# Kernel tuning notes

Hardware: AMD Instinct MI355X
Metric: run time of the kernel (lower is better)

The kernel has to match this reference:

```python
import jax, jax.numpy as jnp
import numpy as np

B, C, H, W = 16, 256, 64, 64
NH, HD, NM = 4, 32, 4  # heads, head_dim, memory tokens
HID = NH * HD


def rms_norm(x, g):
    # F.normalize(x, dim=1) * sqrt(C) * g  (channel dim = 1)
    norm = jnp.maximum(jnp.linalg.norm(x, axis=1, keepdims=True), 1e-12)
    return x / norm * (x.shape[1] ** 0.5) * g


def setup_inputs() -> dict:
    key = jax.random.key(0)
    ks = jax.random.split(key, 5)
    return {
        "x": jax.random.normal(ks[0], (B, C, H, W), jnp.float32),
        "g_in": jnp.ones((1, C, 1, 1), jnp.float32),
        "mem_kv": jax.random.normal(ks[1], (2, NH, HD, NM), jnp.float32),
        "w_qkv": jax.random.normal(ks[2], (HID * 3, C), jnp.float32) * (C ** -0.5),
        "w_out": jax.random.normal(ks[3], (C, HID), jnp.float32) * (HID ** -0.5),
        "b_out": jnp.zeros((C,), jnp.float32),
        "g_out": jnp.ones((1, C, 1, 1), jnp.float32),
    }


def reference(x, g_in, mem_kv, w_qkv, w_out, b_out, g_out):
    b, c, h, w = x.shape
    n = h * w
    scale = HD ** -0.5

    xn = rms_norm(x, g_in)
    # 1x1 conv as matmul over channel dim: [B, 3*HID, H, W]
    qkv = jnp.einsum('oc,bchw->bohw', w_qkv, xn)
    q, k, v = jnp.split(qkv, 3, axis=1)
    # b (h d) x y -> b h d n
    q = q.reshape(b, NH, HD, n)
    k = k.reshape(b, NH, HD, n)
    v = v.reshape(b, NH, HD, n)

    # prepend memory key/value tokens: [b, h, d, NM + n]
    mk = jnp.broadcast_to(mem_kv[0], (b, NH, HD, NM))
    mv = jnp.broadcast_to(mem_kv[1], (b, NH, HD, NM))
    k = jnp.concatenate([mk, k], axis=-1)
    v = jnp.concatenate([mv, v], axis=-1)

    q = jax.nn.softmax(q, axis=-2) * scale  # softmax over head_dim
    k = jax.nn.softmax(k, axis=-1)          # softmax over tokens

    context = jnp.einsum('bhdn,bhen->bhde', k, v)  # [b, h, d, e]
    out = jnp.einsum('bhde,bhdn->bhen', context, q)  # [b, h, e, n]
    out = out.reshape(b, HID, h, w)

    out = jnp.einsum('oc,bchw->bohw', w_out, out) + b_out[None, :, None, None]
    return rms_norm(out, g_out)
```

## Files before the change

kernel.cpp:

```cpp
#include <hip/hip_runtime.h>
#include <math.h>

typedef unsigned short u16;
typedef unsigned int u32;

#define NBATCH 16
#define NCH    256
#define NPIX   4096
#define NHEAD  4
#define HDIM   32
#define NMEM   4
#define HID    128
#define OC3    384
#define SCALE_Q 0.17677669529663687f

typedef __bf16 bf16x8 __attribute__((ext_vector_type(8)));
typedef float  f32x4  __attribute__((ext_vector_type(4)));

__device__ __forceinline__ float bf2f(u16 u){ return __uint_as_float(((u32)u)<<16); }
__device__ __forceinline__ u16 f2bf(float f){
  u32 x = __float_as_uint(f);
  x += 0x7fffu + ((x>>16)&1u);
  return (u16)(x>>16);
}
__device__ __forceinline__ void unpack8(int4 v, float* o){
  u32 a=(u32)v.x, b=(u32)v.y, c=(u32)v.z, d=(u32)v.w;
  o[0]=__uint_as_float(a<<16); o[1]=__uint_as_float(a&0xffff0000u);
  o[2]=__uint_as_float(b<<16); o[3]=__uint_as_float(b&0xffff0000u);
  o[4]=__uint_as_float(c<<16); o[5]=__uint_as_float(c&0xffff0000u);
  o[6]=__uint_as_float(d<<16); o[7]=__uint_as_float(d&0xffff0000u);
}

__global__ __launch_bounds__(256) void k_pack(const float* __restrict__ wqkv,
                                              const float* __restrict__ gin,
                                              const float* __restrict__ wout,
                                              u16* __restrict__ wqb,
                                              u16* __restrict__ wob)
{
  int i = blockIdx.x*256 + threadIdx.x;
  if (i < OC3*NCH){ int c = i & 255; wqb[i] = f2bf(wqkv[i]*gin[c]); }
  else { int j = i - OC3*NCH; wob[j] = f2bf(wout[j]); }
}

__global__ __launch_bounds__(512) void k_qkvx(const float* __restrict__ x,
                                              const u16* __restrict__ wqb,
                                              u16* __restrict__ qkv)
{
  __shared__ u16 BxDs[64*264];
  __shared__ float ssqp[8][64];
  __shared__ float rl[64];
  u16* Ds = BxDs;
  const int t = threadIdx.x, w = t>>6, lane = t&63;
  const int n0 = blockIdx.x*64, b = blockIdx.y;
  const int qw = lane>>4, rr = lane&15;

  {
    const float* xp = x + ((size_t)b*NCH + w*32)*NPIX + n0 + lane;
    float ssq = 0.f;
    #pragma unroll
    for (int j=0;j<4;j++){
      u32 pk[4];
      #pragma unroll
      for (int q=0;q<4;q++){
        float v0 = xp[(size_t)(j*8+2*q  )*NPIX];
        float v1 = xp[(size_t)(j*8+2*q+1)*NPIX];
        ssq += v0*v0 + v1*v1;
        pk[q] = (u32)f2bf(v0) | ((u32)f2bf(v1)<<16);
      }
      *(int4*)&BxDs[lane*264 + w*32 + j*8] = make_int4((int)pk[0],(int)pk[1],(int)pk[2],(int)pk[3]);
    }
    ssqp[w][lane] = ssq;
  }
  __syncthreads();
  if (t < 64){
    float s = 0.f;
    #pragma unroll
    for (int g=0;g<8;g++) s += ssqp[g][t];
    rl[t] = 16.0f / fmaxf(sqrtf(s), 1e-12f);
  }

  f32x4 acc[3][4];
  #pragma unroll
  for (int p=0;p<3;p++)
    #pragma unroll
    for (int nf=0;nf<4;nf++) acc[p][nf] = (f32x4){0.f,0.f,0.f,0.f};

  const u16* a0 = wqb + (size_t)(0*128 + w*16 + rr)*NCH + qw*8;
  const u16* a1 = wqb + (size_t)(1*128 + w*16 + rr)*NCH + qw*8;
  const u16* a2 = wqb + (size_t)(2*128 + w*16 + rr)*NCH + qw*8;
  #pragma unroll
  for (int c0=0; c0<NCH; c0+=32){
    bf16x8 af0 = *(const bf16x8*)(a0 + c0);
    bf16x8 af1 = *(const bf16x8*)(a1 + c0);
    bf16x8 af2 = *(const bf16x8*)(a2 + c0);
    bf16x8 bfr[4];
    #pragma unroll
    for (int nf=0;nf<4;nf++)
      bfr[nf] = *(const bf16x8*)&BxDs[(nf*16+rr)*264 + c0 + qw*8];
    #pragma unroll
    for (int nf=0;nf<4;nf++){
      acc[0][nf] = __builtin_amdgcn_mfma_f32_16x16x32_bf16(af0, bfr[nf], acc[0][nf], 0, 0, 0);
      acc[1][nf] = __builtin_amdgcn_mfma_f32_16x16x32_bf16(af1, bfr[nf], acc[1][nf], 0, 0, 0);
      acc[2][nf] = __builtin_amdgcn_mfma_f32_16x16x32_bf16(af2, bfr[nf], acc[2][nf], 0, 0, 0);
    }
  }

  for (int p=0;p<3;p++){
    __syncthreads();
    #pragma unroll
    for (int nf=0;nf<4;nf++){
      int col = nf*16 + rr;
      float rv = rl[col];
      #pragma unroll
      for (int reg=0;reg<4;reg++){
        int rowl = w*16 + qw*4 + reg;
        Ds[rowl*72 + col] = f2bf(acc[p][nf][reg] * rv);
      }
    }
    __syncthreads();
    if (p==0){
      if (t < 256){
        int h = t>>6, n = t&63;
        float v[32];
        float m = -1e30f;
        #pragma unroll
        for (int d=0;d<32;d++){ v[d] = bf2f(Ds[(h*32+d)*72 + n]); m = fmaxf(m, v[d]); }
        float s = 0.f;
        #pragma unroll
        for (int d=0;d<32;d++){ v[d] = __expf(v[d]-m); s += v[d]; }
        float inv = SCALE_Q / s;
        #pragma unroll
        for (int d=0;d<32;d++) Ds[(h*32+d)*72 + n] = f2bf(v[d]*inv);
      }
      __syncthreads();
    }
    int ro = t>>2, seg = (t&3)*16;
    u16* dst = qkv + ((size_t)(b*OC3 + p*128 + ro))*NPIX + n0 + seg;
    *(int4*)dst     = *(const int4*)&Ds[ro*72 + seg];
    *(int4*)(dst+8) = *(const int4*)&Ds[ro*72 + seg + 8];
  }
}

__global__ __launch_bounds__(256) void k_kred(const u16* __restrict__ qkv,
                                              const float* __restrict__ memkv,
                                              float2* __restrict__ kms,
                                              float* __restrict__ ksm)
{
  const int rid = blockIdx.x*4 + (threadIdx.x>>6);
  const int lane = threadIdx.x & 63;
  const int d = rid & 31, h = (rid>>5)&3, b = rid>>7;
  const u16* p = qkv + (size_t)(b*OC3 + HID + h*HDIM + d)*NPIX;
  u32 buf[32];
  #pragma unroll
  for (int j=0;j<8;j++)
    *(int4*)&buf[j*4] = *(const int4*)(p + (size_t)(j*64+lane)*8);
  float m = -1e30f;
  #pragma unroll
  for (int i=0;i<32;i++){
    float lo = __uint_as_float(buf[i]<<16);
    float hi = __uint_as_float(buf[i]&0xffff0000u);
    m = fmaxf(m, fmaxf(lo, hi));
  }
  float mv[4];
  #pragma unroll
  for (int mm=0;mm<4;mm++){ mv[mm] = memkv[(h*HDIM+d)*NMEM + mm]; m = fmaxf(m, mv[mm]); }
  #pragma unroll
  for (int sh=1; sh<64; sh<<=1) m = fmaxf(m, __shfl_xor(m, sh, 64));
  float ssum = 0.f;
  #pragma unroll
  for (int i=0;i<32;i++){
    float lo = __uint_as_float(buf[i]<<16);
    float hi = __uint_as_float(buf[i]&0xffff0000u);
    ssum += __expf(lo-m) + __expf(hi-m);
  }
  #pragma unroll
  for (int sh=1; sh<64; sh<<=1) ssum += __shfl_xor(ssum, sh, 64);
  #pragma unroll
  for (int mm=0;mm<4;mm++) ssum += __expf(mv[mm]-m);
  float inv = 1.0f/ssum;
  if (lane==0) kms[rid] = make_float2(m, inv);
  if (lane<4) ksm[rid*NMEM + lane] = __expf(mv[lane]-m)*inv;
}

__global__ __launch_bounds__(64) void k_ctx(const u16* __restrict__ qkv,
                                            const float* __restrict__ memkv,
                                            const float* __restrict__ ksm,
                                            const float2* __restrict__ kms,
                                            float* __restrict__ ctxp)
{
  __shared__ float Ks[32][132];
  __shared__ float Vs[32][132];
  const int bh = blockIdx.x;
  const int s  = blockIdx.y;
  const int b = bh>>2, h = bh&3;
  const int t = threadIdx.x;
  const int d0 = (t>>3)*4, e0 = (t&7)*4;
  float acc[4][4] = {};
  if (s==0){
    #pragma unroll
    for (int m=0;m<4;m++){
      float km[4];
      #pragma unroll
      for (int pi=0;pi<4;pi++) km[pi] = ksm[(bh*HDIM + d0+pi)*NMEM + m];
      #pragma unroll
      for (int q=0;q<4;q++){
        float vm = memkv[((NHEAD+h)*HDIM + e0+q)*NMEM + m];
        #pragma unroll
        for (int pi=0;pi<4;pi++) acc[pi][q] += km[pi]*vm;
      }
    }
  }
  const u16* kb = qkv + (size_t)(b*OC3 +   HID + h*HDIM)*NPIX;
  const u16* vb = qkv + (size_t)(b*OC3 + 2*HID + h*HDIM)*NPIX;
  const int lr = t>>1, lseg = (t&1)*64;
  const float2 ms = kms[bh*HDIM + lr];
  const int n0 = s*128;
  {
    const u16* kp = kb + (size_t)lr*NPIX + n0 + lseg;
    const u16* vp = vb + (size_t)lr*NPIX + n0 + lseg;
    #pragma unroll
    for (int u=0;u<8;u++){
      int4 kv = *(const int4*)(kp + u*8);
      int4 vv = *(const int4*)(vp + u*8);
      float kf[8], vf[8];
      unpack8(kv,kf); unpack8(vv,vf);
      #pragma unroll
      for (int i=0;i<8;i++) kf[i] = __expf(kf[i]-ms.x)*ms.y;
      *(float4*)&Ks[lr][lseg+u*8]   = make_float4(kf[0],kf[1],kf[2],kf[3]);
      *(float4*)&Ks[lr][lseg+u*8+4] = make_float4(kf[4],kf[5],kf[6],kf[7]);
      *(float4*)&Vs[lr][lseg+u*8]   = make_float4(vf[0],vf[1],vf[2],vf[3]);
      *(float4*)&Vs[lr][lseg+u*8+4] = make_float4(vf[4],vf[5],vf[6],vf[7]);
    }
    __syncthreads();
    #pragma unroll 4
    for (int nn=0;nn<128;nn+=4){
      float kq[4][4] __attribute__((aligned(16)));
      float vq[4][4] __attribute__((aligned(16)));
      #pragma unroll
      for (int pi=0;pi<4;pi++) *(float4*)kq[pi] = *(const float4*)&Ks[d0+pi][nn];
      #pragma unroll
      for (int q=0;q<4;q++)    *(float4*)vq[q]  = *(const float4*)&Vs[e0+q][nn];
      #pragma unroll
      for (int pi=0;pi<4;pi++)
        #pragma unroll
        for (int q=0;q<4;q++)
          acc[pi][q] += kq[pi][0]*vq[q][0] + kq[pi][1]*vq[q][1]
                      + kq[pi][2]*vq[q][2] + kq[pi][3]*vq[q][3];
    }
  }
  #pragma unroll
  for (int pi=0;pi<4;pi++)
    *(float4*)(ctxp + (size_t)(s*64+bh)*1024 + (d0+pi)*32 + e0) =
      make_float4(acc[pi][0],acc[pi][1],acc[pi][2],acc[pi][3]);
}

__global__ __launch_bounds__(256) void k_ctxred(const float* __restrict__ ctxp,
                                                float* __restrict__ ctx)
{
  const int bh = blockIdx.x, t = threadIdx.x;
  float4 s = make_float4(0.f,0.f,0.f,0.f);
  #pragma unroll
  for (int sp=0; sp<32; sp++){
    float4 v = *(const float4*)(ctxp + (size_t)(sp*64+bh)*1024 + t*4);
    s.x+=v.x; s.y+=v.y; s.z+=v.z; s.w+=v.w;
  }
  *(float4*)(ctx + (size_t)bh*1024 + t*4) = s;
}

__global__ __launch_bounds__(256) void k_fout(const u16* __restrict__ qkv,
                                              const float* __restrict__ ctx,
                                              const u16* __restrict__ wob,
                                              const float* __restrict__ bout,
                                              const float* __restrict__ gout,
                                              float* __restrict__ out)
{
  __shared__ u16 Cb[4*32*40];
  __shared__ u16 Qs[64*136];
  __shared__ u16 Ao[64*136];
  __shared__ float ssql[4][64];
  const int t = threadIdx.x, w = t>>6, lane = t&63;
  const int n0 = blockIdx.x*64, b = blockIdx.y;
  const int qw = lane>>4, rr = lane&15;

  {
    const float4* c4 = (const float4*)(ctx + (size_t)b*4096);
    const int d = (t>>3)&31, e0 = (t&7)*4;
    #pragma unroll
    for (int h=0;h<4;h++){
      float4 v = c4[t + h*256];
      Cb[(h*32+e0+0)*40 + d] = f2bf(v.x);
      Cb[(h*32+e0+1)*40 + d] = f2bf(v.y);
      Cb[(h*32+e0+2)*40 + d] = f2bf(v.z);
      Cb[(h*32+e0+3)*40 + d] = f2bf(v.w);
    }
  }
  {
    const int ro = t>>1, nh = (t&1)*32;
    const u16* qp = qkv + ((size_t)(b*OC3 + ro))*NPIX + n0 + nh;
    u16 tmp[32];
    *(int4*)&tmp[0]  = *(const int4*)(qp);
    *(int4*)&tmp[8]  = *(const int4*)(qp+8);
    *(int4*)&tmp[16] = *(const int4*)(qp+16);
    *(int4*)&tmp[24] = *(const int4*)(qp+24);
    #pragma unroll
    for (int j=0;j<32;j++) Qs[(nh+j)*136 + ro] = tmp[j];
  }
  __syncthreads();

  f32x4 pv[4][2];
  #pragma unroll
  for (int h=0;h<4;h++){
    bf16x8 bq = *(const bf16x8*)&Qs[(w*16+rr)*136 + h*32 + qw*8];
    #pragma unroll
    for (int ef=0;ef<2;ef++){
      bf16x8 af = *(const bf16x8*)&Cb[(h*32 + ef*16 + rr)*40 + qw*8];
      f32x4 z = (f32x4){0.f,0.f,0.f,0.f};
      pv[h][ef] = __builtin_amdgcn_mfma_f32_16x16x32_bf16(af, bq, z, 0, 0, 0);
    }
  }
  #pragma unroll
  for (int h=0;h<4;h++)
    #pragma unroll
    for (int ef=0;ef<2;ef++){
      u32 lohi0 = (u32)f2bf(pv[h][ef][0]) | ((u32)f2bf(pv[h][ef][1])<<16);
      u32 lohi1 = (u32)f2bf(pv[h][ef][2]) | ((u32)f2bf(pv[h][ef][3])<<16);
      *(int2*)&Ao[(w*16+rr)*136 + h*32 + ef*16 + qw*4] = make_int2((int)lohi0,(int)lohi1);
    }
  __syncthreads();

  f32x4 acc[4][4];
  #pragma unroll
  for (int i=0;i<4;i++)
    #pragma unroll
    for (int j=0;j<4;j++) acc[i][j] = (f32x4){0.f,0.f,0.f,0.f};
  #pragma unroll
  for (int k0=0; k0<HID; k0+=32){
    bf16x8 af[4], bfr[4];
    #pragma unroll
    for (int mf=0;mf<4;mf++)
      af[mf] = *(const bf16x8*)&wob[(size_t)(w*64 + mf*16 + rr)*HID + k0 + qw*8];
    #pragma unroll
    for (int nf=0;nf<4;nf++)
      bfr[nf] = *(const bf16x8*)&Ao[(nf*16+rr)*136 + k0 + qw*8];
    #pragma unroll
    for (int mf=0;mf<4;mf++)
      #pragma unroll
      for (int nf=0;nf<4;nf++)
        acc[mf][nf] = __builtin_amdgcn_mfma_f32_16x16x32_bf16(af[mf], bfr[nf], acc[mf][nf], 0, 0, 0);
  }
  float pssq[4] = {0.f,0.f,0.f,0.f};
  #pragma unroll
  for (int mf=0;mf<4;mf++)
    #pragma unroll
    for (int reg=0;reg<4;reg++){
      int c = w*64 + mf*16 + qw*4 + reg;
      float bb = bout[c];
      #pragma unroll
      for (int nf=0;nf<4;nf++){
        float v = acc[mf][nf][reg] + bb;
        acc[mf][nf][reg] = v;
        pssq[nf] += v*v;
      }
    }
  #pragma unroll
  for (int nf=0;nf<4;nf++){
    pssq[nf] += __shfl_xor(pssq[nf], 16, 64);
    pssq[nf] += __shfl_xor(pssq[nf], 32, 64);
  }
  if (qw==0){
    #pragma unroll
    for (int nf=0;nf<4;nf++) ssql[w][nf*16+rr] = pssq[nf];
  }
  __syncthreads();
  float rv[4];
  #pragma unroll
  for (int nf=0;nf<4;nf++){
    int col = nf*16 + rr;
    float sm = ssql[0][col]+ssql[1][col]+ssql[2][col]+ssql[3][col];
    rv[nf] = 16.0f / fmaxf(sqrtf(sm), 1e-12f);
  }
  #pragma unroll
  for (int mf=0;mf<4;mf++)
    #pragma unroll
    for (int reg=0;reg<4;reg++){
      int c = w*64 + mf*16 + qw*4 + reg;
      float g = gout[c];
      float* po = out + ((size_t)(b*NCH + c))*NPIX + n0;
      #pragma unroll
      for (int nf=0;nf<4;nf++)
        po[nf*16 + rr] = acc[mf][nf][reg]*rv[nf]*g;
    }
}

extern "C" void kernel_launch(void* const* d_in, const int* in_sizes, int n_in,
                              void* d_out, int out_size, void* d_ws, size_t ws_size,
                              hipStream_t stream)
{
  const float* x     = (const float*)d_in[0];
  const float* gin   = (const float*)d_in[1];
  const float* memkv = (const float*)d_in[2];
  const float* wqkv  = (const float*)d_in[3];
  const float* wout  = (const float*)d_in[4];
  const float* bout  = (const float*)d_in[5];
  const float* gout  = (const float*)d_in[6];
  float* out = (float*)d_out;

  char* ws = (char*)d_ws;
  u16*    qkv  = (u16*)   (ws);
  float*  ksm  = (float*) (ws + 50331648);
  float2* kms  = (float2*)(ws + 50364416);
  float*  ctxp = (float*) (ws + 50380800);
  float*  ctx  = (float*) (ws + 58769408);
  u16*    wqb  = (u16*)   (ws + 59031552);
  u16*    wob  = (u16*)   (ws + 59228160);

  hipLaunchKernelGGL(k_pack,   dim3(512),   dim3(256), 0, stream, wqkv, gin, wout, wqb, wob);
  hipLaunchKernelGGL(k_qkvx,   dim3(64,16), dim3(512), 0, stream, x, wqb, qkv);
  hipLaunchKernelGGL(k_kred,   dim3(512),   dim3(256), 0, stream, qkv, memkv, kms, ksm);
  hipLaunchKernelGGL(k_ctx,    dim3(64,32), dim3(64),  0, stream, qkv, memkv, ksm, kms, ctxp);
  hipLaunchKernelGGL(k_ctxred, dim3(64),    dim3(256), 0, stream, ctxp, ctx);
  hipLaunchKernelGGL(k_fout,   dim3(64,16), dim3(256), 0, stream, qkv, ctx, wob, bout, gout, out);
}
```

Measured before the change: 200.2 us.

## Write Q token-major and K/V directly from MFMA registers, dropping LDS staging

The QKV projection kernel now writes K and V straight from accumulator registers, swapping MFMA operands so each lane holds contiguous pixels. Q is stored in a separate token-major buffer, and its head-dim softmax is computed in registers with shuffles plus a cross-wave max/sum merge through shared memory. The output kernel then loads Q fragments directly from global memory without a transpose through LDS. This removes several LDS round trips and barriers in both kernels, at the cost of narrower 8-byte global stores and a more intricate two-wave softmax combine.

```diff
diff --git a/kernel.cpp b/kernel.cpp
--- a/kernel.cpp
+++ b/kernel.cpp
@@ -44,12 +44,13 @@
 
 __global__ __launch_bounds__(512) void k_qkvx(const float* __restrict__ x,
                                               const u16* __restrict__ wqb,
-                                              u16* __restrict__ qkv)
-{
-  __shared__ u16 BxDs[64*264];
+                                              u16* __restrict__ qt,
+                                              u16* __restrict__ kv)
+{
+  __shared__ u16 Bx[64*264];
   __shared__ float ssqp[8][64];
+  __shared__ float psx[8][64];
   __shared__ float rl[64];
-  u16* Ds = BxDs;
   const int t = threadIdx.x, w = t>>6, lane = t&63;
   const int n0 = blockIdx.x*64, b = blockIdx.y;
   const int qw = lane>>4, rr = lane&15;
@@ -67,7 +68,7 @@
         ssq += v0*v0 + v1*v1;
         pk[q] = (u32)f2bf(v0) | ((u32)f2bf(v1)<<16);
       }
-      *(int4*)&BxDs[lane*264 + w*32 + j*8] = make_int4((int)pk[0],(int)pk[1],(int)pk[2],(int)pk[3]);
+      *(int4*)&Bx[lane*264 + w*32 + j*8] = make_int4((int)pk[0],(int)pk[1],(int)pk[2],(int)pk[3]);
     }
     ssqp[w][lane] = ssq;
   }
@@ -96,52 +97,67 @@
     bf16x8 bfr[4];
     #pragma unroll
     for (int nf=0;nf<4;nf++)
-      bfr[nf] = *(const bf16x8*)&BxDs[(nf*16+rr)*264 + c0 + qw*8];
+      bfr[nf] = *(const bf16x8*)&Bx[(nf*16+rr)*264 + c0 + qw*8];
     #pragma unroll
     for (int nf=0;nf<4;nf++){
       acc[0][nf] = __builtin_amdgcn_mfma_f32_16x16x32_bf16(af0, bfr[nf], acc[0][nf], 0, 0, 0);
-      acc[1][nf] = __builtin_amdgcn_mfma_f32_16x16x32_bf16(af1, bfr[nf], acc[1][nf], 0, 0, 0);
-      acc[2][nf] = __builtin_amdgcn_mfma_f32_16x16x32_bf16(af2, bfr[nf], acc[2][nf], 0, 0, 0);
-    }
-  }
-
-  for (int p=0;p<3;p++){
-    __syncthreads();
+      acc[1][nf] = __builtin_amdgcn_mfma_f32_16x16x32_bf16(bfr[nf], af1, acc[1][nf], 0, 0, 0);
+      acc[2][nf] = __builtin_amdgcn_mfma_f32_16x16x32_bf16(bfr[nf], af2, acc[2][nf], 0, 0, 0);
+    }
+  }
+
+  __syncthreads();
+
+  #pragma unroll
+  for (int p=1;p<3;p++){
+    u16* base = kv + ((size_t)(b*256 + (p-1)*128 + w*16 + rr))*NPIX + n0;
     #pragma unroll
     for (int nf=0;nf<4;nf++){
-      int col = nf*16 + rr;
-      float rv = rl[col];
-      #pragma unroll
-      for (int reg=0;reg<4;reg++){
-        int rowl = w*16 + qw*4 + reg;
-        Ds[rowl*72 + col] = f2bf(acc[p][nf][reg] * rv);
-      }
-    }
-    __syncthreads();
-    if (p==0){
-      if (t < 256){
-        int h = t>>6, n = t&63;
-        float v[32];
-        float m = -1e30f;
-        #pragma unroll
-        for (int d=0;d<32;d++){ v[d] = bf2f(Ds[(h*32+d)*72 + n]); m = fmaxf(m, v[d]); }
-        float s = 0.f;
-        #pragma unroll
-        for (int d=0;d<32;d++){ v[d] = __expf(v[d]-m); s += v[d]; }
-        float inv = SCALE_Q / s;
-        #pragma unroll
-        for (int d=0;d<32;d++) Ds[(h*32+d)*72 + n] = f2bf(v[d]*inv);
-      }
-      __syncthreads();
-    }
-    int ro = t>>2, seg = (t&3)*16;
-    u16* dst = qkv + ((size_t)(b*OC3 + p*128 + ro))*NPIX + n0 + seg;
-    *(int4*)dst     = *(const int4*)&Ds[ro*72 + seg];
-    *(int4*)(dst+8) = *(const int4*)&Ds[ro*72 + seg + 8];
-  }
-}
-
-__global__ __launch_bounds__(256) void k_kred(const u16* __restrict__ qkv,
+      const float4 rv4 = *(const float4*)&rl[nf*16 + qw*4];
+      u32 lo = (u32)f2bf(acc[p][nf][0]*rv4.x) | ((u32)f2bf(acc[p][nf][1]*rv4.y)<<16);
+      u32 hi = (u32)f2bf(acc[p][nf][2]*rv4.z) | ((u32)f2bf(acc[p][nf][3]*rv4.w)<<16);
+      *(int2*)(base + nf*16 + qw*4) = make_int2((int)lo,(int)hi);
+    }
+  }
+
+  float qv[4][4], pm[4], ps[4];
+  #pragma unroll
+  for (int nf=0;nf<4;nf++){
+    float rv = rl[nf*16 + rr];
+    float m = -1e30f;
+    #pragma unroll
+    for (int r=0;r<4;r++){ qv[nf][r] = acc[0][nf][r]*rv; m = fmaxf(m, qv[nf][r]); }
+    m = fmaxf(m, __shfl_xor(m, 16, 64));
+    m = fmaxf(m, __shfl_xor(m, 32, 64));
+    float s = 0.f;
+    #pragma unroll
+    for (int r=0;r<4;r++){ qv[nf][r] = __expf(qv[nf][r]-m); s += qv[nf][r]; }
+    s += __shfl_xor(s, 16, 64);
+    s += __shfl_xor(s, 32, 64);
+    pm[nf] = m; ps[nf] = s;
+  }
+  if (lane < 16){
+    #pragma unroll
+    for (int nf=0;nf<4;nf++){ ssqp[w][nf*16+lane] = pm[nf]; psx[w][nf*16+lane] = ps[nf]; }
+  }
+  __syncthreads();
+  {
+    const int pw = w^1;
+    u16* qbase = qt + ((size_t)b*NPIX + n0)*HID + w*16 + qw*4;
+    #pragma unroll
+    for (int nf=0;nf<4;nf++){
+      float om = ssqp[pw][nf*16+rr], os = psx[pw][nf*16+rr];
+      float M = fmaxf(pm[nf], om);
+      float S = ps[nf]*__expf(pm[nf]-M) + os*__expf(om-M);
+      float f = __expf(pm[nf]-M) * SCALE_Q / S;
+      u32 lo = (u32)f2bf(qv[nf][0]*f) | ((u32)f2bf(qv[nf][1]*f)<<16);
+      u32 hi = (u32)f2bf(qv[nf][2]*f) | ((u32)f2bf(qv[nf][3]*f)<<16);
+      *(int2*)(qbase + (size_t)(nf*16+rr)*HID) = make_int2((int)lo,(int)hi);
+    }
+  }
+}
+
+__global__ __launch_bounds__(256) void k_kred(const u16* __restrict__ kv,
                                               const float* __restrict__ memkv,
                                               float2* __restrict__ kms,
                                               float* __restrict__ ksm)
@@ -149,7 +165,7 @@
   const int rid = blockIdx.x*4 + (threadIdx.x>>6);
   const int lane = threadIdx.x & 63;
   const int d = rid & 31, h = (rid>>5)&3, b = rid>>7;
-  const u16* p = qkv + (size_t)(b*OC3 + HID + h*HDIM + d)*NPIX;
+  const u16* p = kv + (size_t)(b*256 + h*HDIM + d)*NPIX;
   u32 buf[32];
   #pragma unroll
   for (int j=0;j<8;j++)
@@ -182,7 +198,7 @@
   if (lane<4) ksm[rid*NMEM + lane] = __expf(mv[lane]-m)*inv;
 }
 
-__global__ __launch_bounds__(64) void k_ctx(const u16* __restrict__ qkv,
+__global__ __launch_bounds__(64) void k_ctx(const u16* __restrict__ kv,
                                             const float* __restrict__ memkv,
                                             const float* __restrict__ ksm,
                                             const float2* __restrict__ kms,
@@ -210,8 +226,8 @@
       }
     }
   }
-  const u16* kb = qkv + (size_t)(b*OC3 +   HID + h*HDIM)*NPIX;
-  const u16* vb = qkv + (size_t)(b*OC3 + 2*HID + h*HDIM)*NPIX;
+  const u16* kb = kv + (size_t)(b*256 +       h*HDIM)*NPIX;
+  const u16* vb = kv + (size_t)(b*256 + HID + h*HDIM)*NPIX;
   const int lr = t>>1, lseg = (t&1)*64;
   const float2 ms = kms[bh*HDIM + lr];
   const int n0 = s*128;
@@ -220,10 +236,10 @@
     const u16* vp = vb + (size_t)lr*NPIX + n0 + lseg;
     #pragma unroll
     for (int u=0;u<8;u++){
-      int4 kv = *(const int4*)(kp + u*8);
+      int4 kvv = *(const int4*)(kp + u*8);
       int4 vv = *(const int4*)(vp + u*8);
       float kf[8], vf[8];
-      unpack8(kv,kf); unpack8(vv,vf);
+      unpack8(kvv,kf); unpack8(vv,vf);
       #pragma unroll
       for (int i=0;i<8;i++) kf[i] = __expf(kf[i]-ms.x)*ms.y;
       *(float4*)&Ks[lr][lseg+u*8]   = make_float4(kf[0],kf[1],kf[2],kf[3]);
@@ -267,7 +283,7 @@
   *(float4*)(ctx + (size_t)bh*1024 + t*4) = s;
 }
 
-__global__ __launch_bounds__(256) void k_fout(const u16* __restrict__ qkv,
+__global__ __launch_bounds__(256) void k_fout(const u16* __restrict__ qt,
                                               const float* __restrict__ ctx,
                                               const u16* __restrict__ wob,
                                               const float* __restrict__ bout,
@@ -275,7 +291,6 @@
                                               float* __restrict__ out)
 {
   __shared__ u16 Cb[4*32*40];
-  __shared__ u16 Qs[64*136];
   __shared__ u16 Ao[64*136];
   __shared__ float ssql[4][64];
   const int t = threadIdx.x, w = t>>6, lane = t&63;
@@ -294,23 +309,13 @@
       Cb[(h*32+e0+3)*40 + d] = f2bf(v.w);
     }
   }
-  {
-    const int ro = t>>1, nh = (t&1)*32;
-    const u16* qp = qkv + ((size_t)(b*OC3 + ro))*NPIX + n0 + nh;
-    u16 tmp[32];
-    *(int4*)&tmp[0]  = *(const int4*)(qp);
-    *(int4*)&tmp[8]  = *(const int4*)(qp+8);
-    *(int4*)&tmp[16] = *(const int4*)(qp+16);
-    *(int4*)&tmp[24] = *(const int4*)(qp+24);
-    #pragma unroll
-    for (int j=0;j<32;j++) Qs[(nh+j)*136 + ro] = tmp[j];
-  }
   __syncthreads();
 
   f32x4 pv[4][2];
+  const u16* qp = qt + ((size_t)b*NPIX + n0 + w*16 + rr)*HID;
   #pragma unroll
   for (int h=0;h<4;h++){
-    bf16x8 bq = *(const bf16x8*)&Qs[(w*16+rr)*136 + h*32 + qw*8];
+    bf16x8 bq = *(const bf16x8*)(qp + h*32 + qw*8);
     #pragma unroll
     for (int ef=0;ef<2;ef++){
       bf16x8 af = *(const bf16x8*)&Cb[(h*32 + ef*16 + rr)*40 + qw*8];
@@ -406,7 +411,8 @@
   float* out = (float*)d_out;
 
   char* ws = (char*)d_ws;
-  u16*    qkv  = (u16*)   (ws);
+  u16*    kvb  = (u16*)   (ws);
+  u16*    qt   = (u16*)   (ws + 33554432);
   float*  ksm  = (float*) (ws + 50331648);
   float2* kms  = (float2*)(ws + 50364416);
   float*  ctxp = (float*) (ws + 50380800);
@@ -415,9 +421,9 @@
   u16*    wob  = (u16*)   (ws + 59228160);
 
   hipLaunchKernelGGL(k_pack,   dim3(512),   dim3(256), 0, stream, wqkv, gin, wout, wqb, wob);
-  hipLaunchKernelGGL(k_qkvx,   dim3(64,16), dim3(512), 0, stream, x, wqb, qkv);
-  hipLaunchKernelGGL(k_kred,   dim3(512),   dim3(256), 0, stream, qkv, memkv, kms, ksm);
-  hipLaunchKernelGGL(k_ctx,    dim3(64,32), dim3(64),  0, stream, qkv, memkv, ksm, kms, ctxp);
+  hipLaunchKernelGGL(k_qkvx,   dim3(64,16), dim3(512), 0, stream, x, wqb, qt, kvb);
+  hipLaunchKernelGGL(k_kred,   dim3(512),   dim3(256), 0, stream, kvb, memkv, kms, ksm);
+  hipLaunchKernelGGL(k_ctx,    dim3(64,32), dim3(64),  0, stream, kvb, memkv, ksm, kms, ctxp);
   hipLaunchKernelGGL(k_ctxred, dim3(64),    dim3(256), 0, stream, ctxp, ctx);
-  hipLaunchKernelGGL(k_fout,   dim3(64,16), dim3(256), 0, stream, qkv, ctx, wob, bout, gout, out);
-}
+  hipLaunchKernelGGL(k_fout,   dim3(64,16), dim3(256), 0, stream, qt, ctx, wob, bout, gout, out);
+}
```

Measured after the change: 197.0 us. Within noise of the previous version (-1.6%).
